# Kernel tuning notes

Hardware: AMD Instinct MI355X
Metric: run time of the kernel (lower is better)

## Reference

```python
import jax, jax.numpy as jnp
import numpy as np

C = 32
RES = 512
LEVEL = 6
RADIUS = 2  # half-width of specular filtering window per mip level
_lev_res = [RES >> i for i in range(LEVEL)]
_offsets = np.concatenate([[0], np.cumsum([r * r for r in _lev_res])]).astype(np.int32)
TOTAL = int(_offsets[-1])
_roughness = np.linspace(0.03, 0.99, LEVEL).astype(np.float32)


def _face_dirs(R):
    # unit direction of each texel center on each of the 6 cube faces: (6,R,R,3)
    t = ((np.arange(R) + 0.5) / R * 2.0 - 1.0).astype(np.float32)
    vv, uu = np.meshgrid(t, t, indexing='ij')  # vv: rows (v), uu: cols (u)
    one = np.ones_like(uu)
    f = np.stack([
        np.stack([one, -vv, -uu], -1),   # +x
        np.stack([-one, -vv, uu], -1),   # -x
        np.stack([uu, one, vv], -1),     # +y
        np.stack([uu, -one, -vv], -1),   # -y
        np.stack([uu, -vv, one], -1),    # +z
        np.stack([-uu, -vv, -one], -1)], 0)  # -z
    return (f / np.linalg.norm(f, axis=-1, keepdims=True)).astype(np.float32)

_DIRS = [jnp.asarray(_face_dirs(r)) for r in _lev_res]


def _ggx(cos, alpha):
    a2 = alpha * alpha
    d = a2 / (np.pi * (cos * cos * (a2 - 1.0) + 1.0) ** 2)
    return jnp.where(cos > 0, d, 0.0)


def _specular_filter(feat, dirs, rough):
    # GGX-weighted neighborhood filtering per texel (bounded window = 'specular bound')
    R = feat.shape[-1]
    alpha = float(rough) ** 2
    idx = jnp.arange(R)
    fsum = jnp.zeros_like(feat)
    wsum = jnp.zeros(feat.shape[1:], dtype=feat.dtype)  # (6,R,R)
    for di in range(-RADIUS, RADIUS + 1):
        ii = jnp.clip(idx + di, 0, R - 1)
        for dj in range(-RADIUS, RADIUS + 1):
            jj = jnp.clip(idx + dj, 0, R - 1)
            nd = dirs[:, ii][:, :, jj]                    # (6,R,R,3)
            cos = jnp.clip((dirs * nd).sum(-1), -1.0, 1.0)
            wgt = _ggx(cos, alpha)                        # (6,R,R)
            fsum = fsum + feat[:, :, ii][:, :, :, jj] * wgt[None]
            wsum = wsum + wgt
    return fsum / jnp.maximum(wsum, 1e-8)[None]


def _avg_pool2(x):
    Cc, F, R, _ = x.shape
    return x.reshape(Cc, F, R // 2, 2, R // 2, 2).mean(axis=(3, 5))


def _create_mip(feature):
    pools = [feature.reshape(C, 6, -1)]
    feat = feature
    for i in range(1, LEVEL):
        feat = _avg_pool2(feat)
        pools.append(_specular_filter(feat, _DIRS[i], float(_roughness[i])).reshape(C, 6, -1))
    return jnp.concatenate(pools, axis=-1)  # (C, 6, TOTAL)


def _fetch(mip_pool, w, r):
    # w in [0,1] encodes direction d = 2w-1; pick major-axis cube face, bilinear in face,
    # linear across mip levels selected by roughness r.
    d = w * 2.0 - 1.0
    d = d / jnp.linalg.norm(d, axis=-1, keepdims=True)
    dx, dy, dz = d[:, 0], d[:, 1], d[:, 2]
    ax, ay, az = jnp.abs(dx), jnp.abs(dy), jnp.abs(dz)
    condx = (ax >= ay) & (ax >= az)
    condy = (ay >= az) & (~condx)
    ma = jnp.where(condx, ax, jnp.where(condy, ay, az))
    face = jnp.where(condx, jnp.where(dx > 0, 0, 1),
           jnp.where(condy, jnp.where(dy > 0, 2, 3), jnp.where(dz > 0, 4, 5)))
    u = jnp.where(condx, jnp.where(dx > 0, -dz, dz),
        jnp.where(condy, dx, jnp.where(dz > 0, dx, -dx))) / ma
    v = jnp.where(condx, -dy, jnp.where(condy, jnp.where(dy > 0, dz, -dz), -dy)) / ma
    u01 = (u + 1.0) * 0.5
    v01 = (v + 1.0) * 0.5
    lev_f = jnp.clip((r - _roughness[0]) / (_roughness[-1] - _roughness[0]), 0.0, 1.0) * (LEVEL - 1)
    l0 = jnp.clip(jnp.floor(lev_f).astype(jnp.int32), 0, LEVEL - 1)
    l1 = jnp.minimum(l0 + 1, LEVEL - 1)
    t = lev_f - l0.astype(lev_f.dtype)
    offs = jnp.asarray(_offsets)
    pool_flat = mip_pool.reshape(C, 6 * TOTAL)
    fbase = face.astype(jnp.int32) * TOTAL

    def sample(l):
        res_l = (RES // jnp.left_shift(1, l)).astype(jnp.int32)  # per-query level res
        rf = res_l.astype(u01.dtype)
        x = jnp.clip(u01 * rf - 0.5, 0.0, rf - 1.0)
        y = jnp.clip(v01 * rf - 0.5, 0.0, rf - 1.0)
        x0 = jnp.floor(x).astype(jnp.int32)
        y0 = jnp.floor(y).astype(jnp.int32)
        x1 = jnp.minimum(x0 + 1, res_l - 1)
        y1 = jnp.minimum(y0 + 1, res_l - 1)
        fx = x - x0
        fy = y - y0
        base = fbase + offs[l]
        def g(yy, xx):
            return jnp.take(pool_flat, base + yy * res_l + xx, axis=1)  # (C,B)
        return (g(y0, x0) * (1 - fx) * (1 - fy) + g(y0, x1) * fx * (1 - fy)
              + g(y1, x0) * (1 - fx) * fy + g(y1, x1) * fx * fy)

    out = sample(l0) * (1 - t) + sample(l1) * t  # (C,B)
    return out.T  # (B,C)


def setup_inputs() -> dict:
    key = jax.random.key(0)
    k1, k2, k3 = jax.random.split(key, 3)
    B = 262144
    feature = jax.random.normal(k1, (C, 6, RES, RES), dtype=jnp.float32) * 0.1
    w = jax.random.uniform(k2, (B, 3), dtype=jnp.float32)
    r = jax.random.uniform(k3, (B,), dtype=jnp.float32)
    return {"feature": feature, "w": w, "r": r}


def reference(feature, w, r):
    mip_pool = _create_mip(feature)
    return _fetch(mip_pool, w, r)
```

## Files before the change

kernel.cpp:

```cpp
#include <hip/hip_runtime.h>
#include <cstddef>

#define PI_F 3.14159265358979323846f
#define TOTAL_TEX 349440
#define NC 32
#define LP 257

typedef float nf4 __attribute__((ext_vector_type(4)));

__constant__ int c_offs[6] = {0, 262144, 327680, 344064, 348160, 349184};

static __device__ inline unsigned int f2bf(float x) {
  union { float f; unsigned int u; } v; v.f = x;
  return (v.u + 0x7FFFu + ((v.u >> 16) & 1u)) >> 16;
}
static __device__ inline unsigned int pack2(float lo, float hi) {
  return f2bf(lo) | (f2bf(hi) << 16);
}
static __device__ inline float4 bf4(uint2 q) {
  union { unsigned int u; float f; } a;
  float4 r;
  a.u = q.x << 16;          r.x = a.f;
  a.u = q.x & 0xFFFF0000u;  r.y = a.f;
  a.u = q.y << 16;          r.z = a.f;
  a.u = q.y & 0xFFFF0000u;  r.w = a.f;
  return r;
}
static __device__ inline void bf8(uint4 q, float4& lo, float4& hi) {
  uint2 a, b;
  a.x = q.x; a.y = q.y;
  b.x = q.z; b.y = q.w;
  lo = bf4(a);
  hi = bf4(b);
}

__global__ __launch_bounds__(256) void k_transpose_pool(
    const float* __restrict__ feat, unsigned short* __restrict__ pool0,
    float* __restrict__ pooled1)
{
  __shared__ float tile[32 * LP];
  int blk = blockIdx.x;
  int tx = blk & 7;
  int rem = blk >> 3;
  int ty = rem & 127;
  int f = rem >> 7;
  int gx0 = tx << 6, gy0 = ty << 2;
  int tid = threadIdx.x;
  int lx = tid & 63, ly = tid >> 6;
  int pix = ly * 64 + lx;

  const float* fp = feat + ((size_t)f * 512 + (gy0 + ly)) * 512 + gx0 + lx;
#pragma unroll
  for (int c = 0; c < 32; ++c) {
    tile[c * LP + pix] = fp[(size_t)c * (6 * 512 * 512)];
  }
  __syncthreads();

  size_t rowbase = ((size_t)f * TOTAL_TEX + (size_t)gy0 * 512 + gx0) * NC;
#pragma unroll
  for (int it = 0; it < 8; ++it) {
    int q = it * 256 + tid;
    int texel = q >> 3, cg = q & 7;
    int tyy = texel >> 6, txx = texel & 63;
    float v0 = tile[(cg * 4 + 0) * LP + texel];
    float v1 = tile[(cg * 4 + 1) * LP + texel];
    float v2 = tile[(cg * 4 + 2) * LP + texel];
    float v3 = tile[(cg * 4 + 3) * LP + texel];
    uint2 pk; pk.x = pack2(v0, v1); pk.y = pack2(v2, v3);
    *(uint2*)(pool0 + rowbase + ((size_t)tyy * 512 + txx) * NC + cg * 4) = pk;
  }

  size_t pbase = ((size_t)f * 65536 + (size_t)(gy0 >> 1) * 256 + (gx0 >> 1)) * NC;
#pragma unroll
  for (int it = 0; it < 8; ++it) {
    int e = it * 256 + tid;
    int c = e & 31, px = (e >> 5) & 31, py = e >> 10;
    int b0 = (2 * py) * 64 + 2 * px;
    float v = 0.25f * ((tile[c * LP + b0] + tile[c * LP + b0 + 1]) +
                       (tile[c * LP + b0 + 64] + tile[c * LP + b0 + 65]));
    pooled1[pbase + ((size_t)py * 256 + px) * NC + c] = v;
  }
}

__device__ inline float3 face_dir_norm(int f, int i, int j, float inv2R)
{
  float u = ((float)j + 0.5f) * inv2R - 1.0f;
  float v = ((float)i + 0.5f) * inv2R - 1.0f;
  float x, y, z;
  switch (f) {
    case 0: x = 1.0f;  y = -v; z = -u;   break;
    case 1: x = -1.0f; y = -v; z = u;    break;
    case 2: x = u;  y = 1.0f;  z = v;    break;
    case 3: x = u;  y = -1.0f; z = -v;   break;
    case 4: x = u;  y = -v;    z = 1.0f; break;
    default: x = -u; y = -v;   z = -1.0f; break;
  }
  float s = 1.0f / sqrtf(x * x + y * y + z * z);
  float3 o; o.x = x * s; o.y = y * s; o.z = z * s;
  return o;
}

__global__ __launch_bounds__(256) void k_filter3(
    const float* __restrict__ in, unsigned short* __restrict__ out,
    float* __restrict__ pooled_out,
    int R, int logR, float a2)
{
  __shared__ float wlds[32 * 26];
  __shared__ float4 clds[32][8];
  int tid = threadIdx.x;
  float inv2R = 2.0f / (float)R;

  int txi = blockIdx.x & ((R >> 4) - 1);
  int rest = blockIdx.x >> (logR - 4);
  int tyi = rest & ((R >> 1) - 1);
  int f = rest >> (logR - 1);
  int jbase = txi << 4, ibase = tyi << 1;

  {
    int pl = tid & 31;
    int tg = tid >> 5;
    int j = jbase + (pl & 15);
    int i = ibase + (pl >> 4);
    float3 dc = face_dir_norm(f, i, j, inv2R);
    for (int tap = tg; tap < 25; tap += 8) {
      int di = tap / 5 - 2;
      int dj = tap - (tap / 5) * 5 - 2;
      int ii = min(max(i + di, 0), R - 1);
      int jj = min(max(j + dj, 0), R - 1);
      float3 dn = face_dir_norm(f, ii, jj, inv2R);
      float cs = dc.x * dn.x + dc.y * dn.y + dc.z * dn.z;
      cs = fminf(fmaxf(cs, -1.0f), 1.0f);
      float den = cs * cs * (a2 - 1.0f) + 1.0f;
      float w = (cs > 0.0f) ? (a2 / (PI_F * den * den)) : 0.0f;
      wlds[pl * 26 + tap] = w;
    }
  }
  __syncthreads();

  int cg = tid & 7;
  int pl = tid >> 3;
  int j = jbase + (pl & 15);
  int i = ibase + (pl >> 4);
  const float4* fbase = (const float4*)(in + (((size_t)f << (2 * logR)) * NC));

  float4 acc; acc.x = acc.y = acc.z = acc.w = 0.0f;
  float4 cen; cen.x = cen.y = cen.z = cen.w = 0.0f;
  float wsum = 0.0f;
#pragma unroll
  for (int di = -2; di <= 2; ++di) {
    int ii = min(max(i + di, 0), R - 1);
    int rowb = ii * R;
#pragma unroll
    for (int dj = -2; dj <= 2; ++dj) {
      int jj = min(max(j + dj, 0), R - 1);
      int tap = (di + 2) * 5 + (dj + 2);
      float w = wlds[pl * 26 + tap];
      wsum += w;
      float4 v = fbase[(size_t)(rowb + jj) * 8 + cg];
      if (di == 0 && dj == 0) cen = v;
      acc.x += w * v.x; acc.y += w * v.y; acc.z += w * v.z; acc.w += w * v.w;
    }
  }
  float s = 1.0f / fmaxf(wsum, 1e-8f);
  uint2 pk;
  pk.x = pack2(acc.x * s, acc.y * s);
  pk.y = pack2(acc.z * s, acc.w * s);
  ((uint2*)(out + ((size_t)f * TOTAL_TEX + (size_t)(i * R + j)) * NC))[cg] = pk;

  if (pooled_out) {
    clds[pl][cg] = cen;
    __syncthreads();
    if (tid < 64) {
      int m = tid >> 3;
      int c = tid & 7;
      float4 a = clds[0 * 16 + 2 * m][c];
      float4 b = clds[0 * 16 + 2 * m + 1][c];
      float4 cc = clds[16 + 2 * m][c];
      float4 d = clds[16 + 2 * m + 1][c];
      float4 r;
      r.x = 0.25f * ((a.x + b.x) + (cc.x + d.x));
      r.y = 0.25f * ((a.y + b.y) + (cc.y + d.y));
      r.z = 0.25f * ((a.z + b.z) + (cc.z + d.z));
      r.w = 0.25f * ((a.w + b.w) + (cc.w + d.w));
      int Rp = R >> 1;
      ((float4*)(pooled_out +
                 (((size_t)f * Rp + tyi) * Rp + (txi * 8 + m)) * NC))[c] = r;
    }
  }
}

__global__ __launch_bounds__(256) void k_fetch4(
    const unsigned short* __restrict__ pool, const float* __restrict__ wv,
    const float* __restrict__ rv, float* __restrict__ out, int B)
{
  int t = blockIdx.x * 256 + threadIdx.x;
  int cg = t & 3;
  int b = t >> 2;
  if (b >= B) return;

  float dx = wv[3 * b + 0] * 2.0f - 1.0f;
  float dy = wv[3 * b + 1] * 2.0f - 1.0f;
  float dz = wv[3 * b + 2] * 2.0f - 1.0f;
  float ax = fabsf(dx), ay = fabsf(dy), az = fabsf(dz);
  bool condx = (ax >= ay) && (ax >= az);
  bool condy = (ay >= az) && !condx;
  float ma = condx ? ax : (condy ? ay : az);
  int face = condx ? (dx > 0.0f ? 0 : 1)
                   : (condy ? (dy > 0.0f ? 2 : 3) : (dz > 0.0f ? 4 : 5));
  float un = condx ? (dx > 0.0f ? -dz : dz)
                   : (condy ? dx : (dz > 0.0f ? dx : -dx));
  float vn = condx ? -dy : (condy ? (dy > 0.0f ? dz : -dz) : -dy);
  float u01 = (un / ma + 1.0f) * 0.5f;
  float v01 = (vn / ma + 1.0f) * 0.5f;

  float rr = rv[b];
  float lev_f = fminf(fmaxf((rr - 0.03f) / (0.99f - 0.03f), 0.0f), 1.0f) * 5.0f;
  int l0 = (int)floorf(lev_f);
  l0 = min(max(l0, 0), 5);
  int l1 = min(l0 + 1, 5);
  float tt = lev_f - (float)l0;

  float4 accA; accA.x = accA.y = accA.z = accA.w = 0.0f;
  float4 accB; accB.x = accB.y = accB.z = accB.w = 0.0f;
  int   lvs[2] = {l0, l1};
  float lws[2] = {1.0f - tt, tt};
#pragma unroll
  for (int s = 0; s < 2; ++s) {
    int l = lvs[s];
    float wl = lws[s];
    int res = 512 >> l;
    float rf = (float)res;
    float x = fminf(fmaxf(u01 * rf - 0.5f, 0.0f), rf - 1.0f);
    float y = fminf(fmaxf(v01 * rf - 0.5f, 0.0f), rf - 1.0f);
    int x0 = (int)floorf(x), y0 = (int)floorf(y);
    int x1 = min(x0 + 1, res - 1), y1 = min(y0 + 1, res - 1);
    float fx = x - (float)x0, fy = y - (float)y0;
    const uint4* base16 =
        (const uint4*)(pool + ((size_t)face * TOTAL_TEX + c_offs[l]) * NC);
    float w00 = wl * (1.0f - fx) * (1.0f - fy);
    float w01 = wl * fx * (1.0f - fy);
    float w10 = wl * (1.0f - fx) * fy;
    float w11 = wl * fx * fy;
    uint4 qa = base16[(size_t)(y0 * res + x0) * 4 + cg];
    uint4 qb = base16[(size_t)(y0 * res + x1) * 4 + cg];
    uint4 qc = base16[(size_t)(y1 * res + x0) * 4 + cg];
    uint4 qd = base16[(size_t)(y1 * res + x1) * 4 + cg];
    float4 lo, hi;
    bf8(qa, lo, hi);
    accA.x += w00 * lo.x; accA.y += w00 * lo.y; accA.z += w00 * lo.z; accA.w += w00 * lo.w;
    accB.x += w00 * hi.x; accB.y += w00 * hi.y; accB.z += w00 * hi.z; accB.w += w00 * hi.w;
    bf8(qb, lo, hi);
    accA.x += w01 * lo.x; accA.y += w01 * lo.y; accA.z += w01 * lo.z; accA.w += w01 * lo.w;
    accB.x += w01 * hi.x; accB.y += w01 * hi.y; accB.z += w01 * hi.z; accB.w += w01 * hi.w;
    bf8(qc, lo, hi);
    accA.x += w10 * lo.x; accA.y += w10 * lo.y; accA.z += w10 * lo.z; accA.w += w10 * lo.w;
    accB.x += w10 * hi.x; accB.y += w10 * hi.y; accB.z += w10 * hi.z; accB.w += w10 * hi.w;
    bf8(qd, lo, hi);
    accA.x += w11 * lo.x; accA.y += w11 * lo.y; accA.z += w11 * lo.z; accA.w += w11 * lo.w;
    accB.x += w11 * hi.x; accB.y += w11 * hi.y; accB.z += w11 * hi.z; accB.w += w11 * hi.w;
  }
  nf4* o = (nf4*)(out + (size_t)b * NC);
  nf4 va = {accA.x, accA.y, accA.z, accA.w};
  nf4 vb = {accB.x, accB.y, accB.z, accB.w};
  __builtin_nontemporal_store(va, o + cg * 2);
  __builtin_nontemporal_store(vb, o + cg * 2 + 1);
}

extern "C" void kernel_launch(void* const* d_in, const int* in_sizes, int n_in,
                              void* d_out, int out_size, void* d_ws, size_t ws_size,
                              hipStream_t stream)
{
  const float* feat = (const float*)d_in[0];
  const float* wv   = (const float*)d_in[1];
  const float* rv   = (const float*)d_in[2];
  float* out = (float*)d_out;
  int B = in_sizes[1] / 3;

  unsigned short* pool_t = (unsigned short*)d_ws;
  const size_t POOLT = (size_t)6 * TOTAL_TEX * NC;
  float* pooled1 = (float*)(pool_t + POOLT);
  float* pooled2 = pooled1 + (size_t)6 * 256 * 256 * NC;
  float* pooled3 = pooled2 + (size_t)6 * 128 * 128 * NC;
  float* pooled4 = pooled3 + (size_t)6 * 64 * 64 * NC;
  float* pooled5 = pooled4 + (size_t)6 * 32 * 32 * NC;
  float* pooled[6] = {nullptr, pooled1, pooled2, pooled3, pooled4, pooled5};
  static const int offs[6] = {0, 262144, 327680, 344064, 348160, 349184};

  hipLaunchKernelGGL(k_transpose_pool, dim3(6 * 8 * 128), dim3(256), 0, stream,
                     feat, pool_t, pooled1);

  for (int l = 1; l <= 5; ++l) {
    int R = 512 >> l;
    int logR = 9 - l;
    double rough_d = 0.03 + 0.192 * (double)l;
    float r32 = (float)rough_d;
    double alpha = (double)r32 * (double)r32;
    float a2 = (float)(alpha * alpha);
    int npix = 6 * R * R;
    float* pout = (l < 5) ? pooled[l + 1] : nullptr;
    hipLaunchKernelGGL(k_filter3, dim3(npix / 32), dim3(256), 0, stream,
                       pooled[l], pool_t + (size_t)offs[l] * NC, pout, R, logR, a2);
  }

  hipLaunchKernelGGL(k_fetch4, dim3((B * 4 + 255) / 256), dim3(256), 0, stream,
                     pool_t, wv, rv, out, B);
}
```

Measured before the change: 422.8 us.

## Vectorize transpose tile loads and use one thread per sample in fetch

The transpose kernel now reads the input with float4 loads, four channels per wave, and pads the LDS stride to 260 so the float4 stores stay aligned. The fetch kernel moves from four threads per sample to one thread handling all 32 channels. Each thread issues 16 uint4 loads per level, which removes the repeated direction and weight math per channel group. The trade-offs are higher register pressure, lower occupancy, and a 128-byte per-thread output stride, which makes stores less coalesced.

```diff
diff --git a/kernel.cpp b/kernel.cpp
--- a/kernel.cpp
+++ b/kernel.cpp
@@ -4,7 +4,7 @@
 #define PI_F 3.14159265358979323846f
 #define TOTAL_TEX 349440
 #define NC 32
-#define LP 257
+#define LP 260
 
 typedef float nf4 __attribute__((ext_vector_type(4)));
 
@@ -33,6 +33,9 @@
   lo = bf4(a);
   hi = bf4(b);
 }
+static __device__ inline void fma4(float4& a, float w, float4 v) {
+  a.x += w * v.x; a.y += w * v.y; a.z += w * v.z; a.w += w * v.w;
+}
 
 __global__ __launch_bounds__(256) void k_transpose_pool(
     const float* __restrict__ feat, unsigned short* __restrict__ pool0,
@@ -46,13 +49,20 @@
   int f = rem >> 7;
   int gx0 = tx << 6, gy0 = ty << 2;
   int tid = threadIdx.x;
-  int lx = tid & 63, ly = tid >> 6;
-  int pix = ly * 64 + lx;
-
-  const float* fp = feat + ((size_t)f * 512 + (gy0 + ly)) * 512 + gx0 + lx;
-#pragma unroll
-  for (int c = 0; c < 32; ++c) {
-    tile[c * LP + pix] = fp[(size_t)c * (6 * 512 * 512)];
+
+  {
+    int x4 = tid & 15;
+    int ly = (tid >> 4) & 3;
+    int w  = tid >> 6;
+#pragma unroll
+    for (int p = 0; p < 8; ++p) {
+      int c = p * 4 + w;
+      const float4* src = (const float4*)(
+          feat + (((size_t)c * 6 + f) * 512 + (gy0 + ly)) * 512 + gx0);
+      float4 v = src[x4];
+      int pix = ly * 64 + x4 * 4;
+      *(float4*)&tile[c * LP + pix] = v;
+    }
   }
   __syncthreads();
 
@@ -189,13 +199,11 @@
   }
 }
 
-__global__ __launch_bounds__(256) void k_fetch4(
+__global__ __launch_bounds__(256) void k_fetch1(
     const unsigned short* __restrict__ pool, const float* __restrict__ wv,
     const float* __restrict__ rv, float* __restrict__ out, int B)
 {
-  int t = blockIdx.x * 256 + threadIdx.x;
-  int cg = t & 3;
-  int b = t >> 2;
+  int b = blockIdx.x * 256 + threadIdx.x;
   if (b >= B) return;
 
   float dx = wv[3 * b + 0] * 2.0f - 1.0f;
@@ -220,8 +228,9 @@
   int l1 = min(l0 + 1, 5);
   float tt = lev_f - (float)l0;
 
-  float4 accA; accA.x = accA.y = accA.z = accA.w = 0.0f;
-  float4 accB; accB.x = accB.y = accB.z = accB.w = 0.0f;
+  float4 a0, a1, a2, a3, a4, a5, a6, a7;
+  a0.x=a0.y=a0.z=a0.w=0.f; a1=a0; a2=a0; a3=a0; a4=a0; a5=a0; a6=a0; a7=a0;
+
   int   lvs[2] = {l0, l1};
   float lws[2] = {1.0f - tt, tt};
 #pragma unroll
@@ -241,29 +250,38 @@
     float w01 = wl * fx * (1.0f - fy);
     float w10 = wl * (1.0f - fx) * fy;
     float w11 = wl * fx * fy;
-    uint4 qa = base16[(size_t)(y0 * res + x0) * 4 + cg];
-    uint4 qb = base16[(size_t)(y0 * res + x1) * 4 + cg];
-    uint4 qc = base16[(size_t)(y1 * res + x0) * 4 + cg];
-    uint4 qd = base16[(size_t)(y1 * res + x1) * 4 + cg];
-    float4 lo, hi;
-    bf8(qa, lo, hi);
-    accA.x += w00 * lo.x; accA.y += w00 * lo.y; accA.z += w00 * lo.z; accA.w += w00 * lo.w;
-    accB.x += w00 * hi.x; accB.y += w00 * hi.y; accB.z += w00 * hi.z; accB.w += w00 * hi.w;
-    bf8(qb, lo, hi);
-    accA.x += w01 * lo.x; accA.y += w01 * lo.y; accA.z += w01 * lo.z; accA.w += w01 * lo.w;
-    accB.x += w01 * hi.x; accB.y += w01 * hi.y; accB.z += w01 * hi.z; accB.w += w01 * hi.w;
-    bf8(qc, lo, hi);
-    accA.x += w10 * lo.x; accA.y += w10 * lo.y; accA.z += w10 * lo.z; accA.w += w10 * lo.w;
-    accB.x += w10 * hi.x; accB.y += w10 * hi.y; accB.z += w10 * hi.z; accB.w += w10 * hi.w;
-    bf8(qd, lo, hi);
-    accA.x += w11 * lo.x; accA.y += w11 * lo.y; accA.z += w11 * lo.z; accA.w += w11 * lo.w;
-    accB.x += w11 * hi.x; accB.y += w11 * hi.y; accB.z += w11 * hi.z; accB.w += w11 * hi.w;
-  }
+    size_t t00 = (size_t)(y0 * res + x0) * 4;
+    size_t t01 = (size_t)(y0 * res + x1) * 4;
+    size_t t10 = (size_t)(y1 * res + x0) * 4;
+    size_t t11 = (size_t)(y1 * res + x1) * 4;
+
+#define TAP(OFF, W) do {                                                  \
+    uint4 q0 = base16[(OFF) + 0]; uint4 q1 = base16[(OFF) + 1];           \
+    uint4 q2 = base16[(OFF) + 2]; uint4 q3 = base16[(OFF) + 3];           \
+    float4 lo, hi;                                                        \
+    bf8(q0, lo, hi); fma4(a0, (W), lo); fma4(a1, (W), hi);                \
+    bf8(q1, lo, hi); fma4(a2, (W), lo); fma4(a3, (W), hi);                \
+    bf8(q2, lo, hi); fma4(a4, (W), lo); fma4(a5, (W), hi);                \
+    bf8(q3, lo, hi); fma4(a6, (W), lo); fma4(a7, (W), hi);                \
+  } while (0)
+
+    TAP(t00, w00);
+    TAP(t01, w01);
+    TAP(t10, w10);
+    TAP(t11, w11);
+#undef TAP
+  }
+
   nf4* o = (nf4*)(out + (size_t)b * NC);
-  nf4 va = {accA.x, accA.y, accA.z, accA.w};
-  nf4 vb = {accB.x, accB.y, accB.z, accB.w};
-  __builtin_nontemporal_store(va, o + cg * 2);
-  __builtin_nontemporal_store(vb, o + cg * 2 + 1);
+  nf4 v;
+  v = (nf4){a0.x, a0.y, a0.z, a0.w}; __builtin_nontemporal_store(v, o + 0);
+  v = (nf4){a1.x, a1.y, a1.z, a1.w}; __builtin_nontemporal_store(v, o + 1);
+  v = (nf4){a2.x, a2.y, a2.z, a2.w}; __builtin_nontemporal_store(v, o + 2);
+  v = (nf4){a3.x, a3.y, a3.z, a3.w}; __builtin_nontemporal_store(v, o + 3);
+  v = (nf4){a4.x, a4.y, a4.z, a4.w}; __builtin_nontemporal_store(v, o + 4);
+  v = (nf4){a5.x, a5.y, a5.z, a5.w}; __builtin_nontemporal_store(v, o + 5);
+  v = (nf4){a6.x, a6.y, a6.z, a6.w}; __builtin_nontemporal_store(v, o + 6);
+  v = (nf4){a7.x, a7.y, a7.z, a7.w}; __builtin_nontemporal_store(v, o + 7);
 }
 
 extern "C" void kernel_launch(void* const* d_in, const int* in_sizes, int n_in,
@@ -302,6 +320,6 @@
                        pooled[l], pool_t + (size_t)offs[l] * NC, pout, R, logR, a2);
   }
 
-  hipLaunchKernelGGL(k_fetch4, dim3((B * 4 + 255) / 256), dim3(256), 0, stream,
+  hipLaunchKernelGGL(k_fetch1, dim3((B + 255) / 256), dim3(256), 0, stream,
                      pool_t, wv, rv, out, B);
 }
```

Result: slower. 443.3 us (+4.8%).

## Merge filter levels 2-5 into one launch with separate direct pooling kernel

Applied to the files above, without the earlier changes.

Replaces the five per-level filter launches with a level-1 filter kernel, one pooling kernel that builds levels 3-5 directly from level 2, and a single merged filter kernel whose block index selects level 2-5. This removes serial launch dependencies and gives the small levels, which have few blocks, a fuller grid to share. The cost is that levels 4 and 5 are pooled by re-reading level 2 redundantly. A template parameter also removes the runtime pooling branch.

```diff
diff --git a/kernel.cpp b/kernel.cpp
--- a/kernel.cpp
+++ b/kernel.cpp
@@ -100,18 +100,18 @@
   return o;
 }
 
-__global__ __launch_bounds__(256) void k_filter3(
+template <bool POOL>
+__device__ __forceinline__ void filter_body(
     const float* __restrict__ in, unsigned short* __restrict__ out,
-    float* __restrict__ pooled_out,
-    int R, int logR, float a2)
+    float* __restrict__ pooled_out, int blk, int R, int logR, float a2)
 {
   __shared__ float wlds[32 * 26];
   __shared__ float4 clds[32][8];
   int tid = threadIdx.x;
   float inv2R = 2.0f / (float)R;
 
-  int txi = blockIdx.x & ((R >> 4) - 1);
-  int rest = blockIdx.x >> (logR - 4);
+  int txi = blk & ((R >> 4) - 1);
+  int rest = blk >> (logR - 4);
   int tyi = rest & ((R >> 1) - 1);
   int f = rest >> (logR - 1);
   int jbase = txi << 4, ibase = tyi << 1;
@@ -165,9 +165,9 @@
   uint2 pk;
   pk.x = pack2(acc.x * s, acc.y * s);
   pk.y = pack2(acc.z * s, acc.w * s);
-  ((uint2*)(out + ((size_t)f * TOTAL_TEX + (size_t)(i * R + j)) * NC))[cg] = pk;
-
-  if (pooled_out) {
+  ((uint2*)(out + (size_t)(i * R + j) * NC + (size_t)f * TOTAL_TEX * NC))[cg] = pk;
+
+  if (POOL) {
     clds[pl][cg] = cen;
     __syncthreads();
     if (tid < 64) {
@@ -187,6 +187,82 @@
                  (((size_t)f * Rp + tyi) * Rp + (txi * 8 + m)) * NC))[c] = r;
     }
   }
+}
+
+__global__ __launch_bounds__(256) void k_filter_l1(
+    const float* __restrict__ in, unsigned short* __restrict__ out,
+    float* __restrict__ pooled_out, float a2)
+{
+  filter_body<true>(in, out, pooled_out, blockIdx.x, 256, 8, a2);
+}
+
+__global__ __launch_bounds__(256) void k_pool_rest(
+    const float* __restrict__ p2, float* __restrict__ p3,
+    float* __restrict__ p4, float* __restrict__ p5)
+{
+  const int n3 = 6 * 64 * 64 * 32;
+  const int n4 = 6 * 32 * 32 * 32;
+  int t = blockIdx.x * 256 + threadIdx.x;
+  const int ROW = 128 * 32;
+  if (t < n3) {
+    int c = t & 31, x = (t >> 5) & 63, y = (t >> 11) & 63, f = t >> 17;
+    const float* b = p2 + (((size_t)f * 128 + 2 * y) * 128 + 2 * x) * 32 + c;
+    p3[t] = 0.25f * ((b[0] + b[32]) + (b[ROW] + b[ROW + 32]));
+  } else if (t < n3 + n4) {
+    int t2 = t - n3;
+    int c = t2 & 31, x = (t2 >> 5) & 31, y = (t2 >> 10) & 31, f = t2 >> 15;
+    float q[2][2];
+#pragma unroll
+    for (int sy = 0; sy < 2; ++sy)
+#pragma unroll
+      for (int sx = 0; sx < 2; ++sx) {
+        const float* b = p2 +
+            (((size_t)f * 128 + 4 * y + 2 * sy) * 128 + 4 * x + 2 * sx) * 32 + c;
+        q[sy][sx] = 0.25f * ((b[0] + b[32]) + (b[ROW] + b[ROW + 32]));
+      }
+    p4[t2] = 0.25f * ((q[0][0] + q[0][1]) + (q[1][0] + q[1][1]));
+  } else {
+    int t2 = t - n3 - n4;
+    int c = t2 & 31, x = (t2 >> 5) & 15, y = (t2 >> 9) & 15, f = t2 >> 13;
+    float r[2][2];
+#pragma unroll
+    for (int ry = 0; ry < 2; ++ry)
+#pragma unroll
+      for (int rx = 0; rx < 2; ++rx) {
+        float q[2][2];
+#pragma unroll
+        for (int sy = 0; sy < 2; ++sy)
+#pragma unroll
+          for (int sx = 0; sx < 2; ++sx) {
+            const float* b = p2 +
+                (((size_t)f * 128 + 8 * y + 4 * ry + 2 * sy) * 128 +
+                 8 * x + 4 * rx + 2 * sx) * 32 + c;
+            q[sy][sx] = 0.25f * ((b[0] + b[32]) + (b[ROW] + b[ROW + 32]));
+          }
+        r[ry][rx] = 0.25f * ((q[0][0] + q[0][1]) + (q[1][0] + q[1][1]));
+      }
+    p5[t2] = 0.25f * ((r[0][0] + r[0][1]) + (r[1][0] + r[1][1]));
+  }
+}
+
+__global__ __launch_bounds__(256) void k_filter_merged(
+    const float* __restrict__ pooled2, unsigned short* __restrict__ pool_t,
+    float a2_2, float a2_3, float a2_4, float a2_5)
+{
+  int blk = blockIdx.x;
+  int l, base;
+  float a2;
+  if (blk < 3072)      { l = 2; base = 0;    a2 = a2_2; }
+  else if (blk < 3840) { l = 3; base = 3072; a2 = a2_3; }
+  else if (blk < 4032) { l = 4; base = 3840; a2 = a2_4; }
+  else                 { l = 5; base = 4032; a2 = a2_5; }
+
+  int in_off = (l == 2) ? 0 : (l == 3) ? 3145728 : (l == 4) ? 3932160 : 4128768;
+  int out_off = c_offs[l];
+  int R = 512 >> l;
+  int logR = 9 - l;
+  filter_body<false>(pooled2 + in_off, pool_t + (size_t)out_off * NC,
+                     nullptr, blk - base, R, logR, a2);
 }
 
 __global__ __launch_bounds__(256) void k_fetch4(
@@ -283,24 +359,26 @@
   float* pooled3 = pooled2 + (size_t)6 * 128 * 128 * NC;
   float* pooled4 = pooled3 + (size_t)6 * 64 * 64 * NC;
   float* pooled5 = pooled4 + (size_t)6 * 32 * 32 * NC;
-  float* pooled[6] = {nullptr, pooled1, pooled2, pooled3, pooled4, pooled5};
-  static const int offs[6] = {0, 262144, 327680, 344064, 348160, 349184};
-
-  hipLaunchKernelGGL(k_transpose_pool, dim3(6 * 8 * 128), dim3(256), 0, stream,
-                     feat, pool_t, pooled1);
-
+
+  float a2v[6];
   for (int l = 1; l <= 5; ++l) {
-    int R = 512 >> l;
-    int logR = 9 - l;
     double rough_d = 0.03 + 0.192 * (double)l;
     float r32 = (float)rough_d;
     double alpha = (double)r32 * (double)r32;
-    float a2 = (float)(alpha * alpha);
-    int npix = 6 * R * R;
-    float* pout = (l < 5) ? pooled[l + 1] : nullptr;
-    hipLaunchKernelGGL(k_filter3, dim3(npix / 32), dim3(256), 0, stream,
-                       pooled[l], pool_t + (size_t)offs[l] * NC, pout, R, logR, a2);
-  }
+    a2v[l] = (float)(alpha * alpha);
+  }
+
+  hipLaunchKernelGGL(k_transpose_pool, dim3(6 * 8 * 128), dim3(256), 0, stream,
+                     feat, pool_t, pooled1);
+
+  hipLaunchKernelGGL(k_filter_l1, dim3(6 * 256 * 256 / 32), dim3(256), 0, stream,
+                     pooled1, pool_t + (size_t)262144 * NC, pooled2, a2v[1]);
+
+  hipLaunchKernelGGL(k_pool_rest, dim3(4032), dim3(256), 0, stream,
+                     pooled2, pooled3, pooled4, pooled5);
+
+  hipLaunchKernelGGL(k_filter_merged, dim3(4080), dim3(256), 0, stream,
+                     pooled2, pool_t, a2v[2], a2v[3], a2v[4], a2v[5]);
 
   hipLaunchKernelGGL(k_fetch4, dim3((B * 4 + 255) / 256), dim3(256), 0, stream,
                      pool_t, wv, rv, out, B);
```

Result: no change. 423.7 us (+0.2%).
